# Optimization experiments

Measured on AMD Instinct MI355X. Metric: run time of the kernel, lower is better.

## Reference

```python
import jax, jax.numpy as jnp
import numpy as np

FIN = 4096
N_MEM = 256
SQRT_FIN = 64  # int(FIN ** 0.5)


def setup_inputs() -> dict:
    key = jax.random.key(0)
    ks = jax.random.split(key, 6)
    scale = 0.02  # keep relu-relu scores numerically tame
    x = jax.random.normal(ks[0], (1024, FIN), dtype=jnp.float32)
    Wq = jax.random.normal(ks[1], (FIN, SQRT_FIN * N_MEM), dtype=jnp.float32) * scale
    bq = jnp.zeros((SQRT_FIN * N_MEM,), dtype=jnp.float32)
    Wk = jax.random.normal(ks[2], (FIN, SQRT_FIN * N_MEM), dtype=jnp.float32) * scale
    bk = jnp.zeros((SQRT_FIN * N_MEM,), dtype=jnp.float32)
    v = jax.random.normal(ks[3], (N_MEM, FIN), dtype=jnp.float32) * scale
    Wl = jax.random.normal(ks[4], (FIN, FIN), dtype=jnp.float32) * scale
    bl = jnp.zeros((FIN,), dtype=jnp.float32)
    return {"x": x, "Wq": Wq, "bq": bq, "Wk": Wk, "bk": bk, "v": v, "Wl": Wl, "bl": bl}


def reference(x, Wq, bq, Wk, bk, v, Wl, bl):
    B = x.shape[0]
    # Q/K projections, reshaped to [B, n_mem, sqrt_fin]
    xq = (x @ Wq + bq).reshape(B, N_MEM, SQRT_FIN)
    xk = (x @ Wk + bk).reshape(B, N_MEM, SQRT_FIN)
    # relu-relu score matrix [B, n_mem, n_mem], scaled by sqrt(sqrt_fin)
    scores = jnp.einsum('bms,bns->bmn', jax.nn.relu(xq), jax.nn.relu(xk))
    scores = scores / jnp.sqrt(jnp.asarray(SQRT_FIN, dtype=x.dtype))
    # multiply by learned value memory v [n_mem, fin] (broadcast over batch)
    mem = jnp.einsum('bmn,nf->bmf', scores, v)
    # mean over memory slots, output projection, residual
    pooled = mem.mean(axis=1)  # [B, fin]
    return x + (pooled @ Wl + bl)
```

## Files before the change

kernel.cpp:

```cpp
#include <hip/hip_runtime.h>
#include <hip/hip_bf16.h>
#include <stdint.h>

#define B_SZ 1024
#define FIN  4096
#define NMEM 256
#define NQK  16384

typedef __attribute__((ext_vector_type(8))) short short8;
typedef __attribute__((ext_vector_type(4))) float floatx4;

__device__ __forceinline__ ushort f2bf(float f) {
    uint32_t u = __float_as_uint(f);
    return (ushort)((u + 0x7fffu + ((u >> 16) & 1u)) >> 16);
}
__device__ __forceinline__ float bf2f(ushort u) {
    return __uint_as_float(((uint32_t)u) << 16);
}

__device__ __forceinline__ void gl2lds16(const void* g, void* l) {
    __builtin_amdgcn_global_load_lds(
        (const __attribute__((address_space(1))) void*)g,
        (__attribute__((address_space(3))) void*)l, 16, 0, 0);
}

__global__ void cvt_kernel(const float* __restrict__ src, ushort* __restrict__ dst, int n) {
    int i = (blockIdx.x * blockDim.x + threadIdx.x) * 8;
    if (i >= n) return;
    float4 f0 = *(const float4*)(src + i);
    float4 f1 = *(const float4*)(src + i + 4);
    uint4 o;
    o.x = (uint32_t)f2bf(f0.x) | ((uint32_t)f2bf(f0.y) << 16);
    o.y = (uint32_t)f2bf(f0.z) | ((uint32_t)f2bf(f0.w) << 16);
    o.z = (uint32_t)f2bf(f1.x) | ((uint32_t)f2bf(f1.y) << 16);
    o.w = (uint32_t)f2bf(f1.z) | ((uint32_t)f2bf(f1.w) << 16);
    *(uint4*)(dst + i) = o;
}

__global__ __launch_bounds__(256)
void transT_kernel(const float* __restrict__ src, ushort* __restrict__ dst,
                   int NFULL, int n0) {
    __shared__ float lds[64 * 65];
    const int tid = threadIdx.x;
    const int nc0 = blockIdx.x * 64;
    const int k0  = blockIdx.y * 64;
    #pragma unroll
    for (int p = 0; p < 4; ++p) {
        int idx = p * 256 + tid;
        int krow = idx >> 4;
        int c4 = (idx & 15) * 4;
        float4 v = *(const float4*)(src + (size_t)(k0 + krow) * NFULL + n0 + nc0 + c4);
        lds[krow * 65 + c4 + 0] = v.x;
        lds[krow * 65 + c4 + 1] = v.y;
        lds[krow * 65 + c4 + 2] = v.z;
        lds[krow * 65 + c4 + 3] = v.w;
    }
    __syncthreads();
    #pragma unroll
    for (int p = 0; p < 2; ++p) {
        int idx = p * 256 + tid;
        int nrow = idx >> 3;
        int c8 = (idx & 7) * 8;
        ushort t[8];
        #pragma unroll
        for (int j = 0; j < 8; ++j) t[j] = f2bf(lds[(c8 + j) * 65 + nrow]);
        uint4 o;
        o.x = (uint32_t)t[0] | ((uint32_t)t[1] << 16);
        o.y = (uint32_t)t[2] | ((uint32_t)t[3] << 16);
        o.z = (uint32_t)t[4] | ((uint32_t)t[5] << 16);
        o.w = (uint32_t)t[6] | ((uint32_t)t[7] << 16);
        *(uint4*)(dst + (size_t)(nc0 + nrow) * 4096 + k0 + c8) = o;
    }
}

template<int RELU, int HASBIAS, int RESID, int OUTBF>
__global__ __launch_bounds__(256)
void gemm_bf(const ushort* __restrict__ A, const ushort* __restrict__ Bt,
             const float* __restrict__ bias, const float* __restrict__ resid,
             void* __restrict__ Cout, int ldc, int M, int K)
{
    __shared__ __align__(16) ushort As[128 * 64];
    __shared__ __align__(16) ushort Bs[128 * 64];

    const int tid  = threadIdx.x;
    const int lane = tid & 63;
    const int wave = tid >> 6;
    const int wm = (wave >> 1) * 64;
    const int wn = (wave & 1) * 64;
    const int m0 = blockIdx.y * 128;
    const int n0 = blockIdx.x * 128;

    const int fr = lane & 15;
    const int fq = lane >> 4;

    floatx4 acc[4][4] = {};

    for (int k0 = 0; k0 < K; k0 += 64) {
        __syncthreads();
        #pragma unroll
        for (int i = 0; i < 4; ++i) {
            int id = i * 256 + wave * 64 + lane;
            int row = id >> 3, pos = id & 7;
            int c = pos ^ (row & 7);
            gl2lds16(A + (size_t)(m0 + row) * K + k0 + c * 8,
                     &As[(i * 256 + wave * 64) * 8]);
        }
        #pragma unroll
        for (int i = 0; i < 4; ++i) {
            int id = i * 256 + wave * 64 + lane;
            int row = id >> 3, pos = id & 7;
            int c = pos ^ (row & 7);
            gl2lds16(Bt + (size_t)(n0 + row) * K + k0 + c * 8,
                     &Bs[(i * 256 + wave * 64) * 8]);
        }
        __syncthreads();

        #pragma unroll
        for (int ks = 0; ks < 2; ++ks) {
            short8 a[4], b[4];
            #pragma unroll
            for (int i = 0; i < 4; ++i) {
                int row = wm + i * 16 + fr;
                int p = (ks * 4 + fq) ^ (row & 7);
                a[i] = *(const short8*)(&As[row * 64 + p * 8]);
            }
            #pragma unroll
            for (int i = 0; i < 4; ++i) {
                int row = wn + i * 16 + fr;
                int p = (ks * 4 + fq) ^ (row & 7);
                b[i] = *(const short8*)(&Bs[row * 64 + p * 8]);
            }
            #pragma unroll
            for (int mi = 0; mi < 4; ++mi)
                #pragma unroll
                for (int ni = 0; ni < 4; ++ni)
                    acc[mi][ni] = __builtin_amdgcn_mfma_f32_16x16x32_bf16(
                        a[mi], b[ni], acc[mi][ni], 0, 0, 0);
        }
    }

    #pragma unroll
    for (int mi = 0; mi < 4; ++mi) {
        #pragma unroll
        for (int ni = 0; ni < 4; ++ni) {
            #pragma unroll
            for (int r = 0; r < 4; ++r) {
                int gm = m0 + wm + mi * 16 + fq * 4 + r;
                int gn = n0 + wn + ni * 16 + fr;
                float val = acc[mi][ni][r];
                if (HASBIAS) val += bias[gn];
                if (RELU)    val = fmaxf(val, 0.0f);
                if (RESID)   val += resid[(size_t)gm * ldc + gn];
                if (OUTBF) ((ushort*)Cout)[(size_t)gm * ldc + gn] = f2bf(val);
                else       ((float*)Cout)[(size_t)gm * ldc + gn] = val;
            }
        }
    }
}

#define BM 128
#define BN 128
#define BKK 64
#define LDA 72
#define LDB 72

template<int RELU, int HASBIAS, int RESID, int OUTBF>
__global__ __launch_bounds__(256)
void gemm_k(const ushort* __restrict__ A, const float* __restrict__ B,
            const float* __restrict__ bias, const float* __restrict__ resid,
            void* __restrict__ Cout, int M, int N, int K)
{
    __shared__ ushort As[BM * LDA];
    __shared__ ushort Bs[BN * LDB];

    const int tid  = threadIdx.x;
    const int lane = tid & 63;
    const int wave = tid >> 6;
    const int wm = (wave >> 1) * 64;
    const int wn = (wave & 1) * 64;
    const int m0 = blockIdx.y * BM;
    const int n0 = blockIdx.x * BN;

    const int fr = lane & 15;
    const int fq = lane >> 4;

    floatx4 acc[4][4] = {};

    for (int k0 = 0; k0 < K; k0 += BKK) {
        __syncthreads();
        #pragma unroll
        for (int c = 0; c < 4; ++c) {
            int idx = c * 256 + tid;
            int row = idx >> 3;
            int off = idx & 7;
            *(uint4*)(&As[row * LDA + off * 8]) =
                *(const uint4*)(A + (size_t)(m0 + row) * K + k0 + off * 8);
        }
        #pragma unroll
        for (int p = 0; p < 8; ++p) {
            int idx = p * 256 + tid;
            int nn = idx & 127;
            int kg = idx >> 7;
            const float* bp = B + (size_t)(k0 + kg * 4) * N + n0 + nn;
            float f0 = bp[0];
            float f1 = bp[N];
            float f2 = bp[2 * (size_t)N];
            float f3 = bp[3 * (size_t)N];
            ushort4 w;
            w.x = f2bf(f0); w.y = f2bf(f1); w.z = f2bf(f2); w.w = f2bf(f3);
            *(ushort4*)(&Bs[nn * LDB + kg * 4]) = w;
        }
        __syncthreads();

        #pragma unroll
        for (int ks = 0; ks < 2; ++ks) {
            short8 a[4], b[4];
            #pragma unroll
            for (int i = 0; i < 4; ++i)
                a[i] = *(const short8*)(&As[(wm + i * 16 + fr) * LDA + ks * 32 + fq * 8]);
            #pragma unroll
            for (int i = 0; i < 4; ++i)
                b[i] = *(const short8*)(&Bs[(wn + i * 16 + fr) * LDB + ks * 32 + fq * 8]);
            #pragma unroll
            for (int mi = 0; mi < 4; ++mi)
                #pragma unroll
                for (int ni = 0; ni < 4; ++ni)
                    acc[mi][ni] = __builtin_amdgcn_mfma_f32_16x16x32_bf16(
                        a[mi], b[ni], acc[mi][ni], 0, 0, 0);
        }
    }

    #pragma unroll
    for (int mi = 0; mi < 4; ++mi) {
        #pragma unroll
        for (int ni = 0; ni < 4; ++ni) {
            #pragma unroll
            for (int r = 0; r < 4; ++r) {
                int gm = m0 + wm + mi * 16 + fq * 4 + r;
                int gn = n0 + wn + ni * 16 + fr;
                float val = acc[mi][ni][r];
                if (HASBIAS) val += bias[gn];
                if (RELU)    val = fmaxf(val, 0.0f);
                if (RESID)   val += resid[(size_t)gm * N + gn];
                if (OUTBF) ((ushort*)Cout)[(size_t)gm * N + gn] = f2bf(val);
                else       ((float*)Cout)[(size_t)gm * N + gn] = val;
            }
        }
    }
}

__global__ void qbar_kernel(const ushort* __restrict__ XQr, float* __restrict__ qbar) {
    int b = blockIdx.x;
    int s = threadIdx.x;
    const ushort* p = XQr + (size_t)b * NQK + s;
    float sum = 0.0f;
    #pragma unroll 4
    for (int m = 0; m < NMEM; ++m) sum += bf2f(p[m * 64]);
    qbar[b * 64 + s] = sum * (1.0f / (NMEM * 8.0f));
}

__global__ void spool_kernel(const ushort* __restrict__ XKr, const float* __restrict__ qbar,
                             ushort* __restrict__ spb) {
    int b = blockIdx.x;
    int n = threadIdx.x;
    __shared__ float q[64];
    if (threadIdx.x < 64) q[threadIdx.x] = qbar[b * 64 + threadIdx.x];
    __syncthreads();
    const ushort* p = XKr + (size_t)b * NQK + n * 64;
    float sum = 0.0f;
    #pragma unroll
    for (int s = 0; s < 64; s += 4) {
        ushort4 u = *(const ushort4*)(p + s);
        sum += bf2f(u.x) * q[s] + bf2f(u.y) * q[s + 1]
             + bf2f(u.z) * q[s + 2] + bf2f(u.w) * q[s + 3];
    }
    spb[b * 256 + n] = f2bf(sum);
}

extern "C" void kernel_launch(void* const* d_in, const int* in_sizes, int n_in,
                              void* d_out, int out_size, void* d_ws, size_t ws_size,
                              hipStream_t stream) {
    const float* x  = (const float*)d_in[0];
    const float* Wq = (const float*)d_in[1];
    const float* bq = (const float*)d_in[2];
    const float* Wk = (const float*)d_in[3];
    const float* bk = (const float*)d_in[4];
    const float* v  = (const float*)d_in[5];
    const float* Wl = (const float*)d_in[6];
    const float* bl = (const float*)d_in[7];
    float* out = (float*)d_out;

    const size_t MB = 1ull << 20;
    char* ws = (char*)d_ws;
    ushort* xb   = (ushort*)(ws + 0);
    ushort* XQr  = (ushort*)(ws + 8 * MB);
    ushort* XKr  = (ushort*)(ws + 40 * MB);
    float*  qbar = (float*)(ws + 72 * MB);
    ushort* spb  = (ushort*)(ws + 73 * MB);
    ushort* p2b  = (ushort*)(ws + 74 * MB);
    ushort* WT   = (ushort*)(ws + 82 * MB);

    cvt_kernel<<<dim3((B_SZ * FIN) / 8 / 256), 256, 0, stream>>>(x, xb, B_SZ * FIN);

    for (int c = 0; c < 2; ++c) {
        int n0 = c * 8192;
        transT_kernel<<<dim3(8192 / 64, FIN / 64), 256, 0, stream>>>(Wq, WT, NQK, n0);
        gemm_bf<1, 1, 0, 1><<<dim3(8192 / 128, B_SZ / 128), 256, 0, stream>>>(
            xb, WT, bq + n0, nullptr, XQr + n0, NQK, B_SZ, FIN);
    }
    qbar_kernel<<<dim3(B_SZ), 64, 0, stream>>>(XQr, qbar);

    for (int c = 0; c < 2; ++c) {
        int n0 = c * 8192;
        transT_kernel<<<dim3(8192 / 64, FIN / 64), 256, 0, stream>>>(Wk, WT, NQK, n0);
        gemm_bf<1, 1, 0, 1><<<dim3(8192 / 128, B_SZ / 128), 256, 0, stream>>>(
            xb, WT, bk + n0, nullptr, XKr + n0, NQK, B_SZ, FIN);
    }
    spool_kernel<<<dim3(B_SZ), 256, 0, stream>>>(XKr, qbar, spb);

    gemm_k<0, 0, 0, 1><<<dim3(FIN / BN, B_SZ / BM), 256, 0, stream>>>(
        spb, v, nullptr, nullptr, p2b, B_SZ, FIN, NMEM);

    transT_kernel<<<dim3(FIN / 64, FIN / 64), 256, 0, stream>>>(Wl, WT, FIN, 0);
    gemm_bf<0, 1, 1, 0><<<dim3(FIN / 128, B_SZ / 128), 256, 0, stream>>>(
        p2b, WT, bl, x, out, FIN, B_SZ, FIN);
}
```

Measured before the change: 1.032 ms.

## Merge Q/K projections into one GEMM, pre-transpose weights, swap grid order

Transposes Wq and Wk into a single concatenated bf16 buffer and runs one GEMM over both projections, with a concatenated bias built by device copies. The value memory v is also pre-transposed so the spool→v product reuses the async-LDS gemm_bf kernel instead of the fp32-converting gemm_k. The grid is swapped so blockIdx.x walks M tiles, letting consecutive blocks share the same weight tile in cache. This cuts kernel launches and the chunked transpose/GEMM alternation, at the cost of a larger workspace (about 375 MB).

```diff
diff --git a/kernel.cpp b/kernel.cpp
--- a/kernel.cpp
+++ b/kernel.cpp
@@ -6,6 +6,7 @@
 #define FIN  4096
 #define NMEM 256
 #define NQK  16384
+#define NQK2 32768
 
 typedef __attribute__((ext_vector_type(8))) short short8;
 typedef __attribute__((ext_vector_type(4))) float floatx4;
@@ -39,7 +40,7 @@
 
 __global__ __launch_bounds__(256)
 void transT_kernel(const float* __restrict__ src, ushort* __restrict__ dst,
-                   int NFULL, int n0) {
+                   int NFULL, int n0, int Kd) {
     __shared__ float lds[64 * 65];
     const int tid = threadIdx.x;
     const int nc0 = blockIdx.x * 64;
@@ -69,7 +70,7 @@
         o.y = (uint32_t)t[2] | ((uint32_t)t[3] << 16);
         o.z = (uint32_t)t[4] | ((uint32_t)t[5] << 16);
         o.w = (uint32_t)t[6] | ((uint32_t)t[7] << 16);
-        *(uint4*)(dst + (size_t)(nc0 + nrow) * 4096 + k0 + c8) = o;
+        *(uint4*)(dst + (size_t)(nc0 + nrow) * Kd + k0 + c8) = o;
     }
 }
 
@@ -77,7 +78,7 @@
 __global__ __launch_bounds__(256)
 void gemm_bf(const ushort* __restrict__ A, const ushort* __restrict__ Bt,
              const float* __restrict__ bias, const float* __restrict__ resid,
-             void* __restrict__ Cout, int ldc, int M, int K)
+             void* __restrict__ Cout, int ldc, int K)
 {
     __shared__ __align__(16) ushort As[128 * 64];
     __shared__ __align__(16) ushort Bs[128 * 64];
@@ -87,8 +88,8 @@
     const int wave = tid >> 6;
     const int wm = (wave >> 1) * 64;
     const int wn = (wave & 1) * 64;
-    const int m0 = blockIdx.y * 128;
-    const int n0 = blockIdx.x * 128;
+    const int m0 = blockIdx.x * 128;
+    const int n0 = blockIdx.y * 128;
 
     const int fr = lane & 15;
     const int fq = lane >> 4;
@@ -158,115 +159,24 @@
     }
 }
 
-#define BM 128
-#define BN 128
-#define BKK 64
-#define LDA 72
-#define LDB 72
-
-template<int RELU, int HASBIAS, int RESID, int OUTBF>
-__global__ __launch_bounds__(256)
-void gemm_k(const ushort* __restrict__ A, const float* __restrict__ B,
-            const float* __restrict__ bias, const float* __restrict__ resid,
-            void* __restrict__ Cout, int M, int N, int K)
-{
-    __shared__ ushort As[BM * LDA];
-    __shared__ ushort Bs[BN * LDB];
-
-    const int tid  = threadIdx.x;
-    const int lane = tid & 63;
-    const int wave = tid >> 6;
-    const int wm = (wave >> 1) * 64;
-    const int wn = (wave & 1) * 64;
-    const int m0 = blockIdx.y * BM;
-    const int n0 = blockIdx.x * BN;
-
-    const int fr = lane & 15;
-    const int fq = lane >> 4;
-
-    floatx4 acc[4][4] = {};
-
-    for (int k0 = 0; k0 < K; k0 += BKK) {
-        __syncthreads();
-        #pragma unroll
-        for (int c = 0; c < 4; ++c) {
-            int idx = c * 256 + tid;
-            int row = idx >> 3;
-            int off = idx & 7;
-            *(uint4*)(&As[row * LDA + off * 8]) =
-                *(const uint4*)(A + (size_t)(m0 + row) * K + k0 + off * 8);
-        }
-        #pragma unroll
-        for (int p = 0; p < 8; ++p) {
-            int idx = p * 256 + tid;
-            int nn = idx & 127;
-            int kg = idx >> 7;
-            const float* bp = B + (size_t)(k0 + kg * 4) * N + n0 + nn;
-            float f0 = bp[0];
-            float f1 = bp[N];
-            float f2 = bp[2 * (size_t)N];
-            float f3 = bp[3 * (size_t)N];
-            ushort4 w;
-            w.x = f2bf(f0); w.y = f2bf(f1); w.z = f2bf(f2); w.w = f2bf(f3);
-            *(ushort4*)(&Bs[nn * LDB + kg * 4]) = w;
-        }
-        __syncthreads();
-
-        #pragma unroll
-        for (int ks = 0; ks < 2; ++ks) {
-            short8 a[4], b[4];
-            #pragma unroll
-            for (int i = 0; i < 4; ++i)
-                a[i] = *(const short8*)(&As[(wm + i * 16 + fr) * LDA + ks * 32 + fq * 8]);
-            #pragma unroll
-            for (int i = 0; i < 4; ++i)
-                b[i] = *(const short8*)(&Bs[(wn + i * 16 + fr) * LDB + ks * 32 + fq * 8]);
-            #pragma unroll
-            for (int mi = 0; mi < 4; ++mi)
-                #pragma unroll
-                for (int ni = 0; ni < 4; ++ni)
-                    acc[mi][ni] = __builtin_amdgcn_mfma_f32_16x16x32_bf16(
-                        a[mi], b[ni], acc[mi][ni], 0, 0, 0);
-        }
-    }
-
-    #pragma unroll
-    for (int mi = 0; mi < 4; ++mi) {
-        #pragma unroll
-        for (int ni = 0; ni < 4; ++ni) {
-            #pragma unroll
-            for (int r = 0; r < 4; ++r) {
-                int gm = m0 + wm + mi * 16 + fq * 4 + r;
-                int gn = n0 + wn + ni * 16 + fr;
-                float val = acc[mi][ni][r];
-                if (HASBIAS) val += bias[gn];
-                if (RELU)    val = fmaxf(val, 0.0f);
-                if (RESID)   val += resid[(size_t)gm * N + gn];
-                if (OUTBF) ((ushort*)Cout)[(size_t)gm * N + gn] = f2bf(val);
-                else       ((float*)Cout)[(size_t)gm * N + gn] = val;
-            }
-        }
-    }
-}
-
-__global__ void qbar_kernel(const ushort* __restrict__ XQr, float* __restrict__ qbar) {
+__global__ void qbar_kernel(const ushort* __restrict__ XQK, float* __restrict__ qbar) {
     int b = blockIdx.x;
     int s = threadIdx.x;
-    const ushort* p = XQr + (size_t)b * NQK + s;
+    const ushort* p = XQK + (size_t)b * NQK2 + s;
     float sum = 0.0f;
     #pragma unroll 4
     for (int m = 0; m < NMEM; ++m) sum += bf2f(p[m * 64]);
     qbar[b * 64 + s] = sum * (1.0f / (NMEM * 8.0f));
 }
 
-__global__ void spool_kernel(const ushort* __restrict__ XKr, const float* __restrict__ qbar,
+__global__ void spool_kernel(const ushort* __restrict__ XQK, const float* __restrict__ qbar,
                              ushort* __restrict__ spb) {
     int b = blockIdx.x;
     int n = threadIdx.x;
     __shared__ float q[64];
     if (threadIdx.x < 64) q[threadIdx.x] = qbar[b * 64 + threadIdx.x];
     __syncthreads();
-    const ushort* p = XKr + (size_t)b * NQK + n * 64;
+    const ushort* p = XQK + (size_t)b * NQK2 + NQK + n * 64;
     float sum = 0.0f;
     #pragma unroll
     for (int s = 0; s < 64; s += 4) {
@@ -293,35 +203,33 @@
     const size_t MB = 1ull << 20;
     char* ws = (char*)d_ws;
     ushort* xb   = (ushort*)(ws + 0);
-    ushort* XQr  = (ushort*)(ws + 8 * MB);
-    ushort* XKr  = (ushort*)(ws + 40 * MB);
-    float*  qbar = (float*)(ws + 72 * MB);
-    ushort* spb  = (ushort*)(ws + 73 * MB);
-    ushort* p2b  = (ushort*)(ws + 74 * MB);
-    ushort* WT   = (ushort*)(ws + 82 * MB);
+    ushort* WT   = (ushort*)(ws + 8 * MB);
+    ushort* WlT  = (ushort*)(ws + 264 * MB);
+    ushort* vT   = (ushort*)(ws + 296 * MB);
+    ushort* XQK  = (ushort*)(ws + 300 * MB);
+    float*  qbar = (float*)(ws + 364 * MB);
+    ushort* spb  = (ushort*)(ws + 365 * MB);
+    ushort* p2b  = (ushort*)(ws + 366 * MB);
+    float*  bcat = (float*)(ws + 374 * MB);
+
+    hipMemcpyAsync(bcat,         bq, NQK * sizeof(float), hipMemcpyDeviceToDevice, stream);
+    hipMemcpyAsync(bcat + NQK,   bk, NQK * sizeof(float), hipMemcpyDeviceToDevice, stream);
 
     cvt_kernel<<<dim3((B_SZ * FIN) / 8 / 256), 256, 0, stream>>>(x, xb, B_SZ * FIN);
-
-    for (int c = 0; c < 2; ++c) {
-        int n0 = c * 8192;
-        transT_kernel<<<dim3(8192 / 64, FIN / 64), 256, 0, stream>>>(Wq, WT, NQK, n0);
-        gemm_bf<1, 1, 0, 1><<<dim3(8192 / 128, B_SZ / 128), 256, 0, stream>>>(
-            xb, WT, bq + n0, nullptr, XQr + n0, NQK, B_SZ, FIN);
-    }
-    qbar_kernel<<<dim3(B_SZ), 64, 0, stream>>>(XQr, qbar);
-
-    for (int c = 0; c < 2; ++c) {
-        int n0 = c * 8192;
-        transT_kernel<<<dim3(8192 / 64, FIN / 64), 256, 0, stream>>>(Wk, WT, NQK, n0);
-        gemm_bf<1, 1, 0, 1><<<dim3(8192 / 128, B_SZ / 128), 256, 0, stream>>>(
-            xb, WT, bk + n0, nullptr, XKr + n0, NQK, B_SZ, FIN);
-    }
-    spool_kernel<<<dim3(B_SZ), 256, 0, stream>>>(XKr, qbar, spb);
-
-    gemm_k<0, 0, 0, 1><<<dim3(FIN / BN, B_SZ / BM), 256, 0, stream>>>(
-        spb, v, nullptr, nullptr, p2b, B_SZ, FIN, NMEM);
-
-    transT_kernel<<<dim3(FIN / 64, FIN / 64), 256, 0, stream>>>(Wl, WT, FIN, 0);
-    gemm_bf<0, 1, 1, 0><<<dim3(FIN / 128, B_SZ / 128), 256, 0, stream>>>(
-        p2b, WT, bl, x, out, FIN, B_SZ, FIN);
-}
+    transT_kernel<<<dim3(NQK / 64, FIN / 64), 256, 0, stream>>>(Wq, WT, NQK, 0, FIN);
+    transT_kernel<<<dim3(NQK / 64, FIN / 64), 256, 0, stream>>>(Wk, WT + (size_t)NQK * FIN, NQK, 0, FIN);
+    transT_kernel<<<dim3(FIN / 64, FIN / 64), 256, 0, stream>>>(Wl, WlT, FIN, 0, FIN);
+    transT_kernel<<<dim3(FIN / 64, NMEM / 64), 256, 0, stream>>>(v, vT, FIN, 0, NMEM);
+
+    gemm_bf<1, 1, 0, 1><<<dim3(B_SZ / 128, NQK2 / 128), 256, 0, stream>>>(
+        xb, WT, bcat, nullptr, XQK, NQK2, FIN);
+
+    qbar_kernel<<<dim3(B_SZ), 64, 0, stream>>>(XQK, qbar);
+    spool_kernel<<<dim3(B_SZ), 256, 0, stream>>>(XQK, qbar, spb);
+
+    gemm_bf<0, 0, 0, 1><<<dim3(B_SZ / 128, FIN / 128), 256, 0, stream>>>(
+        spb, vT, nullptr, nullptr, p2b, FIN, NMEM);
+
+    gemm_bf<0, 1, 1, 0><<<dim3(B_SZ / 128, FIN / 128), 256, 0, stream>>>(
+        p2b, WlT, bl, x, out, FIN, FIN);
+}
```

Result: slower. 1.154 ms (+11.8%).
